# Kernel tuning notes

Measured on AMD Instinct MI355X. Metric: run time of the kernel, lower is better.

Reference implementation:

```python
import jax, jax.numpy as jnp
import numpy as np
from jax import lax

B, C, H, W = 8, 256, 64, 64
O, K, E = 256, 3, 3  # out_channels, kernel_size, num_experts

def setup_inputs() -> dict:
    key = jax.random.key(0)
    k1, k2, k3, k4, k5 = jax.random.split(key, 5)
    q = jax.random.normal(k1, (B, C, H, W), dtype=jnp.float32)
    y = jax.random.normal(k2, (B, C, H, W), dtype=jnp.float32)
    experts = jax.random.normal(k3, (E, O, 2 * C, K, K), dtype=jnp.float32)
    # torch nn.Linear(2C, E): store transposed [2C, E] for ctx @ gate_w
    bound = 1.0 / np.sqrt(2 * C)
    gate_w = jax.random.uniform(k4, (2 * C, E), minval=-bound, maxval=bound, dtype=jnp.float32)
    gate_b = jax.random.uniform(k5, (E,), minval=-bound, maxval=bound, dtype=jnp.float32)
    return {"q": q, "y": y, "experts": experts, "gate_w": gate_w, "gate_b": gate_b}

def reference(q, y, experts, gate_w, gate_b):
    # gate: softmax over experts from global-avg-pooled context of y (duplicated)
    y_ctx = jnp.mean(y, axis=(2, 3))                       # [B, C]
    context = jnp.concatenate([y_ctx, y_ctx], axis=1)       # [B, 2C]
    gates = jax.nn.softmax(context @ gate_w + gate_b, axis=1)  # [B, E]
    # per-sample fused kernel: sum_e gates[b,e] * experts[e]  -> [B, O, 2C, K, K]
    w = jnp.einsum('be,eoikl->boikl', gates, experts)
    xy = jnp.concatenate([q, q], axis=1)                     # [B, 2C, H, W]
    # batched dynamic conv via grouped conv: batch -> groups (no Python loop)
    b, c2, h, wd = xy.shape
    x1 = xy.reshape(1, b * c2, h, wd)
    w1 = w.reshape(b * O, c2, K, K)
    out = lax.conv_general_dilated(
        x1, w1, window_strides=(1, 1), padding='SAME',
        dimension_numbers=('NCHW', 'OIHW', 'NCHW'),
        feature_group_count=b)
    return out.reshape(b, O, h, wd)
```

## Files before the change

kernel.cpp:

```cpp
#include <hip/hip_runtime.h>
#include <hip/hip_bf16.h>
#include <math.h>


typedef __bf16 bf16x8 __attribute__((ext_vector_type(8)));
typedef __bf16 bf16x4 __attribute__((ext_vector_type(4)));
typedef float f32x4 __attribute__((ext_vector_type(4)));

#define AS1 __attribute__((address_space(1)))
#define AS3 __attribute__((address_space(3)))

__global__ __launch_bounds__(64) void yctx_kernel(const float* __restrict__ y,
                                                  float* __restrict__ yctx) {
  int bc = blockIdx.x;
  const float4* p = (const float4*)(y + (size_t)bc * 4096);
  int lane = threadIdx.x;
  float s = 0.f;
  for (int i = lane; i < 1024; i += 64) {
    float4 v = p[i];
    s += v.x + v.y + v.z + v.w;
  }
#pragma unroll
  for (int off = 32; off > 0; off >>= 1) s += __shfl_down(s, off, 64);
  if (lane == 0) yctx[bc] = s * (1.f / 4096.f);
}

union PrepSmem {
  struct {
    float sf[3][2304];
    float lg[8][3];
    float g[8][3];
  } wb;
  float tile2[64][33];
};

__global__ __launch_bounds__(256) void prep_kernel(const float* __restrict__ q,
                                                   const float* __restrict__ experts,
                                                   const float* __restrict__ yctx,
                                                   const float* __restrict__ gw,
                                                   const float* __restrict__ gb,
                                                   __bf16* __restrict__ qT,
                                                   __bf16* __restrict__ wf) {
  __shared__ PrepSmem sm;
  int bid = blockIdx.x;
  int tid = threadIdx.x;

  if (bid < 256) {
    int o = bid;

    {
      int lb = tid >> 5, li = tid & 31;
      float p0 = 0.f, p1 = 0.f, p2 = 0.f;
#pragma unroll
      for (int j = 0; j < 8; j++) {
        int c = li + j * 32;
        float yv = yctx[lb * 256 + c];
        p0 += yv * (gw[c * 3 + 0] + gw[(c + 256) * 3 + 0]);
        p1 += yv * (gw[c * 3 + 1] + gw[(c + 256) * 3 + 1]);
        p2 += yv * (gw[c * 3 + 2] + gw[(c + 256) * 3 + 2]);
      }
#pragma unroll
      for (int off = 16; off > 0; off >>= 1) {
        p0 += __shfl_down(p0, off, 32);
        p1 += __shfl_down(p1, off, 32);
        p2 += __shfl_down(p2, off, 32);
      }
      if (li == 0) {
        sm.wb.lg[lb][0] = p0 + gb[0];
        sm.wb.lg[lb][1] = p1 + gb[1];
        sm.wb.lg[lb][2] = p2 + gb[2];
      }
    }

#pragma unroll
    for (int e = 0; e < 3; e++) {
      const float4* src = (const float4*)(experts + ((size_t)e * 256 + o) * 4608);
      float4* dstp = (float4*)sm.wb.sf[e];
      for (int i = tid; i < 576; i += 256) {
        float4 a = src[i], bq = src[i + 576];
        float4 r;
        r.x = a.x + bq.x; r.y = a.y + bq.y; r.z = a.z + bq.z; r.w = a.w + bq.w;
        dstp[i] = r;
      }
    }
    __syncthreads();
    if (tid < 8) {
      float l0 = sm.wb.lg[tid][0], l1 = sm.wb.lg[tid][1], l2 = sm.wb.lg[tid][2];
      float m = fmaxf(l0, fmaxf(l1, l2));
      float e0 = __expf(l0 - m), e1 = __expf(l1 - m), e2 = __expf(l2 - m);
      float inv = 1.f / (e0 + e1 + e2);
      sm.wb.g[tid][0] = e0 * inv; sm.wb.g[tid][1] = e1 * inv; sm.wb.g[tid][2] = e2 * inv;
    }
    __syncthreads();

    int cl = tid & 31, ch = tid >> 5;
    size_t lbase = (size_t)ch * 8192 + (size_t)(o >> 4) * 512 +
                   (size_t)((cl >> 3) * 128) + (size_t)((o & 15) * 8) + (cl & 7);
#pragma unroll 1
    for (int b = 0; b < 8; b++) {
      float g0 = sm.wb.g[b][0], g1 = sm.wb.g[b][1], g2 = sm.wb.g[b][2];
#pragma unroll
      for (int tap = 0; tap < 9; tap++) {
        float v = g0 * sm.wb.sf[0][tid * 9 + tap] + g1 * sm.wb.sf[1][tid * 9 + tap] +
                  g2 * sm.wb.sf[2][tid * 9 + tap];
        wf[((size_t)b * 9 + tap) * 65536 + lbase] = (__bf16)v;
      }
    }
    return;
  }

  int bid2 = bid - 256;
  int hp = bid2 % 66;
  int t2 = bid2 / 66;
  int ch = t2 & 7;
  int b = t2 >> 3;
  __bf16* dst = qT + (((size_t)(b * 8 + ch) * 66 + hp) * 66) * 32;
  float4 z4 = {0.f, 0.f, 0.f, 0.f};
  if (hp == 0 || hp == 65) {
    float4* d4 = (float4*)dst;
    for (int i = tid; i < 264; i += 256) d4[i] = z4;
    return;
  }
  int h = hp - 1;
  {
    int w = tid & 63, ci = tid >> 6;
#pragma unroll
    for (int j = 0; j < 8; j++) {
      int c = ci * 8 + j;
      sm.tile2[w][c] = q[(((size_t)b * 256 + ch * 32 + c) * 64 + h) * 64 + w];
    }
  }
  if (tid < 4) ((float4*)dst)[tid] = z4;
  else if (tid < 8) ((float4*)(dst + 65 * 32))[tid - 4] = z4;
  __syncthreads();

  int a = tid & 7, wsl = tid >> 3;
  int cl4 = a * 4;
#pragma unroll
  for (int k = 0; k < 2; k++) {
    int w = wsl * 2 + k, wp = w + 1;
    int clp4 = (((cl4 >> 3) ^ ((wp >> 1) & 3)) << 3) | (cl4 & 7);
    float v0 = sm.tile2[w][cl4 + 0], v1 = sm.tile2[w][cl4 + 1];
    float v2 = sm.tile2[w][cl4 + 2], v3 = sm.tile2[w][cl4 + 3];
    bf16x4 r = {(__bf16)v0, (__bf16)v1, (__bf16)v2, (__bf16)v3};
    *(bf16x4*)(dst + wp * 32 + clp4) = r;
  }
}

__global__ __launch_bounds__(512, 2) void conv_kernel(const __bf16* __restrict__ qT,
                                                      const __bf16* __restrict__ wf,
                                                      float* __restrict__ out) {
  __shared__ __align__(16) __bf16 Qlds[2][6 * 66 * 32];
  const int tid = threadIdx.x;
  const int lane = tid & 63;
  const int wv = tid >> 6;
  const int wm = wv >> 2;
  const int wn = wv & 3;
  const int l15 = lane & 15, qd = lane >> 4;

  const int bid = blockIdx.x;
  const int b = bid & 7;
  const int rem = bid >> 3;
  const int o0 = (rem >> 4) * 128;
  const int hq = (rem & 15) * 4;

  f32x4 acc[4][4];
  {
    f32x4 z = {0.f, 0.f, 0.f, 0.f};
#pragma unroll
    for (int i = 0; i < 4; i++)
#pragma unroll
      for (int j = 0; j < 4; j++) acc[i][j] = z;
  }

  const char* qT_b = (const char*)qT + (size_t)b * 8 * 66 * 66 * 32 * 2;
  const char* abase = (const char*)wf + (size_t)b * 9 * 8 * 16384 +
                      (size_t)(o0 + wm * 64) * 64 + (size_t)lane * 16;
  bf16x8 areg[3][4];

  {
    const char* qsrc = qT_b + ((size_t)hq) * 66 * 32 * 2;
    for (int i = tid; i < 1584; i += 512) {
      int ub = i - lane;
      __builtin_amdgcn_global_load_lds((const AS1 void*)(qsrc + ((size_t)i << 4)),
                                       (AS3 void*)((char*)Qlds[0] + ((size_t)ub << 4)),
                                       16, 0, 0);
    }
#pragma unroll
    for (int mi = 0; mi < 4; mi++) {
      areg[0][mi] = *(const bf16x8*)(abase + mi * 1024);
      areg[1][mi] = *(const bf16x8*)(abase + ((size_t)8 << 14) + mi * 1024);
    }
    __syncthreads();
  }

#pragma unroll 1
  for (int ch = 0; ch < 8; ch++) {
    const char* Qb = (const char*)Qlds[ch & 1];
    const char* qsrc_n = qT_b + ((size_t)(ch + 1) * 66 + hq) * 66 * 32 * 2;
    char* qdst_n = (char*)Qlds[(ch + 1) & 1];
#pragma unroll
    for (int tap = 0; tap < 9; tap++) {
      {
        int tapn = (tap + 2 >= 9) ? tap - 7 : tap + 2;
        int chn = (tap + 2 >= 9) ? ch + 1 : ch;
        size_t aoff = ((size_t)(tapn * 8 + chn)) << 14;
#pragma unroll
        for (int mi = 0; mi < 4; mi++)
          areg[(tap + 2) % 3][mi] = *(const bf16x8*)(abase + aoff + mi * 1024);
      }
      if (ch < 7) {
        if (tap == 0) {
          for (int i = tid; i < 792; i += 512) {
            int ub = i - lane;
            __builtin_amdgcn_global_load_lds((const AS1 void*)(qsrc_n + ((size_t)i << 4)),
                                             (AS3 void*)(qdst_n + ((size_t)ub << 4)),
                                             16, 0, 0);
          }
        } else if (tap == 1) {
          for (int i = 792 + tid; i < 1584; i += 512) {
            int ub = i - lane;
            __builtin_amdgcn_global_load_lds((const AS1 void*)(qsrc_n + ((size_t)i << 4)),
                                             (AS3 void*)(qdst_n + ((size_t)ub << 4)),
                                             16, 0, 0);
          }
        }
      }
      const int dh = tap / 3, dw = tap - dh * 3;
      const int r = wn + dh;
#pragma unroll
      for (int ni = 0; ni < 4; ni++) {
        int wp = ni * 16 + l15 + dw;
        int g = (qd ^ ((wp >> 1) & 3)) << 3;
        bf16x8 bfv = *(const bf16x8*)(Qb + ((r * 66 + wp) * 32 + g) * 2);
#pragma unroll
        for (int mi = 0; mi < 4; mi++)
          acc[mi][ni] = __builtin_amdgcn_mfma_f32_16x16x32_bf16(
              areg[tap % 3][mi], bfv, acc[mi][ni], 0, 0, 0);
      }
    }
    __syncthreads();
  }

  const int hh = hq + wn;
#pragma unroll
  for (int mi = 0; mi < 4; mi++) {
    int o = o0 + wm * 64 + mi * 16 + qd * 4;
#pragma unroll
    for (int ni = 0; ni < 4; ni++) {
      int w = ni * 16 + l15;
#pragma unroll
      for (int rr = 0; rr < 4; rr++)
        out[(((size_t)b * 256 + (o + rr)) * 64 + hh) * 64 + w] = acc[mi][ni][rr];
    }
  }
}

extern "C" void kernel_launch(void* const* d_in, const int* in_sizes, int n_in,
                              void* d_out, int out_size, void* d_ws, size_t ws_size,
                              hipStream_t stream) {
  (void)in_sizes; (void)n_in; (void)out_size; (void)ws_size;
  const float* q = (const float*)d_in[0];
  const float* y = (const float*)d_in[1];
  const float* experts = (const float*)d_in[2];
  const float* gate_w = (const float*)d_in[3];
  const float* gate_b = (const float*)d_in[4];
  float* out = (float*)d_out;

  char* ws = (char*)d_ws;
  float* yctx = (float*)ws;
  __bf16* wf = (__bf16*)(ws + 16384);
  __bf16* qT = (__bf16*)(ws + 16384 + 9437184);

  yctx_kernel<<<2048, 64, 0, stream>>>(y, yctx);
  prep_kernel<<<256 + 4224, 256, 0, stream>>>(q, experts, yctx, gate_w, gate_b, qT, wf);
  conv_kernel<<<256, 512, 0, stream>>>(qT, wf, out);
}
```

Before: 170.2 us.

## Widen yctx reduction blocks and vectorize expert-weight folding writes

The y-context reduction now uses 256-thread blocks with a shared-memory cross-wave sum instead of one wave per channel. The weight-prep blocks are reorganized so each block handles 16 output channels by a channel slice, staging folded expert weights in padded shared memory. It then writes 8 contiguous bf16 values per store rather than scalar 2-byte stores. This is meant to cut uncoalesced global stores and raise occupancy in prep, in exchange for more complex indexing and strided shared-memory reads.

```diff
diff --git a/kernel.cpp b/kernel.cpp
--- a/kernel.cpp
+++ b/kernel.cpp
@@ -10,24 +10,28 @@
 #define AS1 __attribute__((address_space(1)))
 #define AS3 __attribute__((address_space(3)))
 
-__global__ __launch_bounds__(64) void yctx_kernel(const float* __restrict__ y,
-                                                  float* __restrict__ yctx) {
+__global__ __launch_bounds__(256) void yctx_kernel(const float* __restrict__ y,
+                                                   float* __restrict__ yctx) {
   int bc = blockIdx.x;
   const float4* p = (const float4*)(y + (size_t)bc * 4096);
-  int lane = threadIdx.x;
+  int tid = threadIdx.x;
   float s = 0.f;
-  for (int i = lane; i < 1024; i += 64) {
-    float4 v = p[i];
+#pragma unroll
+  for (int k = 0; k < 4; k++) {
+    float4 v = p[tid + k * 256];
     s += v.x + v.y + v.z + v.w;
   }
 #pragma unroll
   for (int off = 32; off > 0; off >>= 1) s += __shfl_down(s, off, 64);
-  if (lane == 0) yctx[bc] = s * (1.f / 4096.f);
+  __shared__ float wsum[4];
+  if ((tid & 63) == 0) wsum[tid >> 6] = s;
+  __syncthreads();
+  if (tid == 0) yctx[bc] = (wsum[0] + wsum[1] + wsum[2] + wsum[3]) * (1.f / 4096.f);
 }
 
 union PrepSmem {
   struct {
-    float sf[3][2304];
+    float sfold[3 * 16 * 145];
     float lg[8][3];
     float g[8][3];
   } wb;
@@ -46,7 +50,9 @@
   int tid = threadIdx.x;
 
   if (bid < 256) {
-    int o = bid;
+    int og = bid >> 4, chh = bid & 15;
+    int chb = chh >> 1;
+    int qb = (chh & 1) * 2;
 
     {
       int lb = tid >> 5, li = tid & 31;
@@ -72,16 +78,15 @@
       }
     }
 
-#pragma unroll
-    for (int e = 0; e < 3; e++) {
-      const float4* src = (const float4*)(experts + ((size_t)e * 256 + o) * 4608);
-      float4* dstp = (float4*)sm.wb.sf[e];
-      for (int i = tid; i < 576; i += 256) {
-        float4 a = src[i], bq = src[i + 576];
-        float4 r;
-        r.x = a.x + bq.x; r.y = a.y + bq.y; r.z = a.z + bq.z; r.w = a.w + bq.w;
-        dstp[i] = r;
-      }
+    for (int i = tid; i < 1728; i += 256) {
+      int p = i / 36, f = i - p * 36;
+      int e = p >> 4, olp = p & 15;
+      int o = og * 16 + olp;
+      const float4* src = (const float4*)experts + ((size_t)(e * 256 + o)) * 1152 + chh * 36;
+      float4 lo = src[f], hi = src[f + 576];
+      float* dst = &sm.wb.sfold[p * 145 + f * 4];
+      dst[0] = lo.x + hi.x; dst[1] = lo.y + hi.y;
+      dst[2] = lo.z + hi.z; dst[3] = lo.w + hi.w;
     }
     __syncthreads();
     if (tid < 8) {
@@ -93,17 +98,24 @@
     }
     __syncthreads();
 
-    int cl = tid & 31, ch = tid >> 5;
-    size_t lbase = (size_t)ch * 8192 + (size_t)(o >> 4) * 512 +
-                   (size_t)((cl >> 3) * 128) + (size_t)((o & 15) * 8) + (cl & 7);
 #pragma unroll 1
     for (int b = 0; b < 8; b++) {
       float g0 = sm.wb.g[b][0], g1 = sm.wb.g[b][1], g2 = sm.wb.g[b][2];
-#pragma unroll
-      for (int tap = 0; tap < 9; tap++) {
-        float v = g0 * sm.wb.sf[0][tid * 9 + tap] + g1 * sm.wb.sf[1][tid * 9 + tap] +
-                  g2 * sm.wb.sf[2][tid * 9 + tap];
-        wf[((size_t)b * 9 + tap) * 65536 + lbase] = (__bf16)v;
+      for (int i = tid; i < 288; i += 256) {
+        int tap = i >> 5, ck = i & 31;
+        int qdl = ck >> 4, ol = ck & 15;
+        const float* r0 = &sm.wb.sfold[(0 * 16 + ol) * 145 + (qdl * 8) * 9 + tap];
+        const float* r1 = &sm.wb.sfold[(1 * 16 + ol) * 145 + (qdl * 8) * 9 + tap];
+        const float* r2 = &sm.wb.sfold[(2 * 16 + ol) * 145 + (qdl * 8) * 9 + tap];
+        bf16x8 rv;
+#pragma unroll
+        for (int j = 0; j < 8; j++) {
+          float v = g0 * r0[j * 9] + g1 * r1[j * 9] + g2 * r2[j * 9];
+          rv[j] = (__bf16)v;
+        }
+        size_t byteoff = (((size_t)b * 9 + tap) * 8 + chb) * 16384 +
+                         (size_t)og * 1024 + (size_t)(qb + qdl) * 256 + (size_t)ol * 16;
+        *(bf16x8*)((char*)wf + byteoff) = rv;
       }
     }
     return;
@@ -272,7 +284,7 @@
   __bf16* wf = (__bf16*)(ws + 16384);
   __bf16* qT = (__bf16*)(ws + 16384 + 9437184);
 
-  yctx_kernel<<<2048, 64, 0, stream>>>(y, yctx);
+  yctx_kernel<<<2048, 256, 0, stream>>>(y, yctx);
   prep_kernel<<<256 + 4224, 256, 0, stream>>>(q, experts, yctx, gate_w, gate_b, qT, wf);
   conv_kernel<<<256, 512, 0, stream>>>(qT, wf, out);
 }
```

New measurement: 158.4 us. 1.07x faster.
